# Optimization experiments

Measured on AMD Instinct MI355X. Metric: run time of the kernel, lower is better.

Reference implementation:

```python
import jax, jax.numpy as jnp
import numpy as np

DT = 0.1
B_SZ = 8192
T_HIST = 20
LEN_PRED = 30
FEAT = 32
N_LAYERS = 3
# state transition for constant-acceleration model (matches self.F in torch)
F_MAT = np.array([[1.0, DT, DT * DT / 2], [0.0, 1.0, DT], [0.0, 0.0, 1.0]], dtype=np.float32)


def setup_inputs() -> dict:
    key = jax.random.key(0)
    ks = jax.random.split(key, 16)
    # random-walk trajectories as history observations
    hist = jnp.cumsum(jax.random.normal(ks[0], (B_SZ, T_HIST, 2), jnp.float32) * 0.5, axis=1)
    k_lin = 1.0 / np.sqrt(FEAT)
    k_in = 1.0 / np.sqrt(24)

    def u(k, shape, scale):
        return jax.random.uniform(k, shape, jnp.float32, -scale, scale)

    return {
        "hist": hist,
        "max_accel_x": jnp.ones((1,), jnp.float32) * 10.0,
        "max_accel_y": jnp.ones((1,), jnp.float32) * 20.0,
        "velocity_std_x": jnp.ones((1,), jnp.float32) * 10.0,
        "acceleration_std_x": jnp.ones((1,), jnp.float32) * 10.0,
        "R_x_": jnp.array([0.0448], jnp.float32),
        "R_y_": jnp.array([0.001], jnp.float32),
        "G_x": jnp.array([0.0059, 0.2981, 0.0393], jnp.float32),
        "G_y": jnp.array([0.0059, 0.2981, 0.0393], jnp.float32) / 5.0,
        "Win_W": u(ks[1], (FEAT, 24), k_in),
        "Win_b": u(ks[2], (FEAT,), k_in),
        "enc_Wih": u(ks[3], (N_LAYERS, 4 * FEAT, FEAT), k_lin),
        "enc_Whh": u(ks[4], (N_LAYERS, 4 * FEAT, FEAT), k_lin),
        "enc_bih": u(ks[5], (N_LAYERS, 4 * FEAT), k_lin),
        "enc_bhh": u(ks[6], (N_LAYERS, 4 * FEAT), k_lin),
        "dec_Wih": u(ks[7], (N_LAYERS, 4 * FEAT, FEAT), k_lin),
        "dec_Whh": u(ks[8], (N_LAYERS, 4 * FEAT, FEAT), k_lin),
        "dec_bih": u(ks[9], (N_LAYERS, 4 * FEAT), k_lin),
        "dec_bhh": u(ks[10], (N_LAYERS, 4 * FEAT), k_lin),
        "Wout_W": u(ks[11], (4, FEAT), k_lin),
        "Wout_b": u(ks[12], (4,), k_lin),
        "len_pred": LEN_PRED,
    }


def reference(hist, max_accel_x, max_accel_y, velocity_std_x, acceleration_std_x,
              R_x_, R_y_, G_x, G_y, Win_W, Win_b,
              enc_Wih, enc_Whh, enc_bih, enc_bhh,
              dec_Wih, dec_Whh, dec_bih, dec_bhh,
              Wout_W, Wout_b, len_pred):
    B = hist.shape[0]
    F = jnp.asarray(F_MAT)
    R_x = R_x_[0] * R_x_[0]
    R_y = R_y_[0] * R_y_[0]
    Z_x = hist[:, :, 0]
    Z_y = hist[:, :, 1]

    def lstm(x, h, c, Wih, Whh, bih, bhh):
        g = x @ Wih.T + bih + h @ Whh.T + bhh
        i, f, gg, o = jnp.split(g, 4, axis=1)
        c = jax.nn.sigmoid(f) * c + jax.nn.sigmoid(i) * jnp.tanh(gg)
        h = jax.nn.sigmoid(o) * jnp.tanh(c)
        return h, c

    def stack(XP, h, c, Wih, Whh, bih, bhh):
        x = jnp.tanh(XP @ Win_W.T + Win_b)
        hs, cs = [], []
        for j in range(N_LAYERS):
            hj, cj = lstm(x, h[j], c[j], Wih[j], Whh[j], bih[j], bhh[j])
            hs.append(hj)
            cs.append(cj)
            x = cj  # torch code feeds the fresh CELL state to the next layer
        return jnp.stack(hs), jnp.stack(cs)

    def kpred(X, P, Q):
        return X @ F.T, jnp.einsum('ij,bjk,lk->bil', F, P, F) + Q

    def kupdate(X, P, z, R):
        y = z - X[:, 0]                      # innovation (H picks component 0)
        S = P[:, 0, 0] + R                   # innovation covariance (scalar)
        K = P[:, :, 0] / S[:, None]          # Kalman gain (B,3)
        return X + y[:, None] * K, P - K[:, :, None] * P[:, 0:1, :]

    def kinit(z0):
        # torch always calls _kalman_init with is_x=True (default), so both
        # axes use R_x / velocity_std_x / acceleration_std_x
        X = jnp.zeros((B, 3), hist.dtype).at[:, 0].set(z0)
        d = jnp.stack([R_x, velocity_std_x[0] ** 2, acceleration_std_x[0] ** 2])
        P = jnp.zeros((B, 3, 3), hist.dtype).at[:, jnp.arange(3), jnp.arange(3)].set(d)
        return X, P

    Qx_e = jnp.outer(G_x * max_accel_x[0], G_x * max_accel_x[0])
    Qy_e = jnp.outer(G_y * max_accel_y[0], G_y * max_accel_y[0])

    Xx, Px = kinit(Z_x[:, 0])
    Xy, Py = kinit(Z_y[:, 0])
    h = jnp.zeros((N_LAYERS, B, FEAT), hist.dtype)
    c = jnp.zeros_like(h)

    def enc_step(carry, zs):
        Xx, Px, Xy, Py, h, c = carry
        zx, zy = zs
        XP = jnp.concatenate([Xx, Xy, Px.reshape(B, 9), Py.reshape(B, 9)], 1)
        h, c = stack(XP, h, c, enc_Wih, enc_Whh, enc_bih, enc_bhh)
        Xx, Px = kpred(Xx, Px, Qx_e)
        Xy, Py = kpred(Xy, Py, Qy_e)
        Xx, Px = kupdate(Xx, Px, zx, R_x)
        Xy, Py = kupdate(Xy, Py, zy, R_y)
        return (Xx, Px, Xy, Py, h, c), None

    carry, _ = jax.lax.scan(enc_step, (Xx, Px, Xy, Py, h, c),
                            (Z_x[:, 1:].T, Z_y[:, 1:].T))

    oxx = jnp.outer(G_x, G_x)
    oyy = jnp.outer(G_y, G_y)

    def dec_step(carry, _):
        Xx, Px, Xy, Py, h, c = carry
        XP = jnp.concatenate([Xx, Xy, Px.reshape(B, 9), Py.reshape(B, 9)], 1)
        h, c = stack(XP, h, c, dec_Wih, dec_Whh, dec_bih, dec_bhh)
        pred = c[-1] @ Wout_W.T + Wout_b  # (B,4): [u_x, u_y, std_x, std_y]
        Xx = Xx.at[:, 2].set(DT * pred[:, 0])  # X[:,2] = B*u
        Xy = Xy.at[:, 2].set(DT * pred[:, 1])
        Qx = (pred[:, 2] ** 2)[:, None, None] * oxx
        Qy = (pred[:, 3] ** 2)[:, None, None] * oyy
        Xx, Px = kpred(Xx, Px, Qx)
        Xy, Py = kpred(Xy, Py, Qy)
        out = jnp.stack([Xx[:, 0], Xy[:, 0],
                         jnp.sqrt(Px[:, 0, 0]), jnp.sqrt(Py[:, 0, 0]),
                         jnp.zeros(B, hist.dtype)], axis=1)  # (B,5)
        return (Xx, Px, Xy, Py, h, c), out

    carry, ys = jax.lax.scan(dec_step, carry, None, length=len_pred)
    return jnp.transpose(ys, (1, 0, 2))  # (B, len_pred, 5)
```

## Files before the change

### kernel.cpp

```cpp
#include <hip/hip_runtime.h>
#include <math.h>

#define DT   0.1f
#define HDT  0.005f
#define T_HIST 20
#define LEN_PRED 30

typedef __attribute__((ext_vector_type(8))) short bfrag8;
typedef __attribute__((ext_vector_type(4))) float f32x4;

#define WS_FRAG   0u
#define WS_WIN    98304u
#define WS_WOUT   100352u
#define WS_BIAS   101376u

static __device__ __forceinline__ unsigned short f2bf(float x) {
    union { float f; unsigned int u; } v; v.f = x;
    unsigned int r = v.u + 0x7fffu + ((v.u >> 16) & 1u);
    return (unsigned short)(r >> 16);
}

static __device__ __forceinline__ unsigned int cvtpk(float lo, float hi) {
    unsigned int r;
    asm("v_cvt_pk_bf16_f32 %0, %1, %2" : "=v"(r) : "v"(lo), "v"(hi));
    return r;
}

__global__ void prep_kernel(const float* __restrict__ Win_W,
                            const float* __restrict__ eWih, const float* __restrict__ eWhh,
                            const float* __restrict__ ebih, const float* __restrict__ ebhh,
                            const float* __restrict__ dWih, const float* __restrict__ dWhh,
                            const float* __restrict__ dbih, const float* __restrict__ dbhh,
                            const float* __restrict__ Wout_W,
                            char* __restrict__ ws)
{
    int i = blockIdx.x * blockDim.x + threadIdx.x;
    if (i < 49152) {
        int fi = i >> 9, within = i & 511;
        int lane = within >> 3, jj = within & 7;
        int t = fi & 7, c = (fi >> 3) & 1;
        int pl = fi >> 4;
        int l = pl % 3, ph = pl / 3;
        int p = lane & 15, q2 = lane >> 4;
        int gate = p & 3;
        int feat = 8 * (p >> 2) + t;
        int row = gate * 32 + feat;
        int k = q2 * 8 + jj;
        const float* W = (c == 0) ? (ph ? dWih : eWih) : (ph ? dWhh : eWhh);
        ((unsigned short*)(ws + WS_FRAG))[i] = f2bf(W[l * 4096 + row * 32 + k]);
    } else if (i < 50176) {
        int i2 = i - 49152;
        int t = i2 >> 9, within = i2 & 511;
        int lane = within >> 3, jj = within & 7;
        int p = lane & 15, q2 = lane >> 4;
        int feat = 8 * (p >> 2) + 4 * t + (p & 3);
        int k = q2 * 8 + jj;
        float v = (k < 24) ? Win_W[feat * 24 + k] : 0.f;
        ((unsigned short*)(ws + WS_WIN))[i2] = f2bf(v);
    } else if (i < 50688) {
        int i3 = i - 50176;
        int lane = i3 >> 3, jj = i3 & 7;
        int p = lane & 15, q2 = lane >> 4;
        float v = Wout_W[(p & 3) * 32 + q2 * 8 + jj];
        ((unsigned short*)(ws + WS_WOUT))[i3] = f2bf(v);
    } else if (i < 51456) {
        int b = i - 50688;
        int ph = b / 384, rem = b % 384;
        int l = rem >> 7, w2 = rem & 127;
        int col = w2 >> 2, r = w2 & 3;
        const float* bi = ph ? dbih : ebih;
        const float* bh = ph ? dbhh : ebhh;
        ((float*)(ws + WS_BIAS))[b] = bi[l * 128 + r * 32 + col] + bh[l * 128 + r * 32 + col];
    }
}

__launch_bounds__(256, 2)
__global__ void kalman_lstm_kernel(const float* __restrict__ hist,
                                   const float* __restrict__ max_ax, const float* __restrict__ max_ay,
                                   const float* __restrict__ vstd, const float* __restrict__ astd,
                                   const float* __restrict__ Rx_, const float* __restrict__ Ry_,
                                   const float* __restrict__ Gx, const float* __restrict__ Gy,
                                   const float* __restrict__ Win_b, const float* __restrict__ Wout_b,
                                   const char* __restrict__ ws, float* __restrict__ out)
{
    __shared__ __align__(16) unsigned int xchC[3][2][4][16][4];
    __shared__ __align__(16) unsigned int xchH[3][2][4][16][4];
    __shared__ __align__(16) bfrag8 xenc[T_HIST - 1][64];

    const int tid  = threadIdx.x;
    const int wv   = tid >> 6;
    const int lane = tid & 63;
    const int q    = lane >> 4;
    const int m    = lane & 15;
    const int be   = blockIdx.x * 16 + m;
    const f32x4 zero4 = {0.f, 0.f, 0.f, 0.f};

    const bfrag8* fragp = (const bfrag8*)(ws + WS_FRAG);
    const f32x4*  biasp = (const f32x4*)(ws + WS_BIAS);

    bfrag8 fragA[3][2][2];
    f32x4  biasV[3][2];
    auto load_phase = [&](int ph) {
#pragma unroll
        for (int l = 0; l < 3; ++l) {
#pragma unroll
            for (int c = 0; c < 2; ++c)
#pragma unroll
                for (int j = 0; j < 2; ++j)
                    fragA[l][c][j] = fragp[(((ph * 3 + l) * 2 + c) * 8 + (2 * wv + j)) * 64 + lane];
#pragma unroll
            for (int j = 0; j < 2; ++j)
                biasV[l][j] = biasp[ph * 96 + l * 32 + (8 * q + 2 * wv + j)];
        }
    };

    bfrag8 winF0 = ((const bfrag8*)(ws + WS_WIN))[lane];
    bfrag8 winF1 = ((const bfrag8*)(ws + WS_WIN))[64 + lane];
    f32x4 winBv[2];
#pragma unroll
    for (int t = 0; t < 2; ++t)
#pragma unroll
        for (int r = 0; r < 4; ++r) winBv[t][r] = Win_b[8 * q + 4 * t + r];
    bfrag8 woutF = ((const bfrag8*)(ws + WS_WOUT))[lane];
    const float wb0 = Wout_b[0], wb1 = Wout_b[1], wb2 = Wout_b[2], wb3 = Wout_b[3];

    const float rx = Rx_[0] * Rx_[0], ry = Ry_[0] * Ry_[0];
    const float gX0 = Gx[0], gX1 = Gx[1], gX2 = Gx[2];
    const float gY0 = Gy[0], gY1 = Gy[1], gY2 = Gy[2];
    const float gx00 = gX0*gX0, gx01 = gX0*gX1, gx02 = gX0*gX2,
                gx11 = gX1*gX1, gx12 = gX1*gX2, gx22 = gX2*gX2;
    const float gy00 = gY0*gY0, gy01 = gY0*gY1, gy02 = gY0*gY2,
                gy11 = gY1*gY1, gy12 = gY1*gY2, gy22 = gY2*gY2;
    const float sx2 = max_ax[0] * max_ax[0], sy2 = max_ay[0] * max_ay[0];

    float Xx0 = hist[be * 40 + 0], Xx1 = 0.f, Xx2 = 0.f;
    float Xy0 = hist[be * 40 + 1], Xy1 = 0.f, Xy2 = 0.f;
    const float pv = vstd[0] * vstd[0], pa = astd[0] * astd[0];
    float Px00 = rx, Px01 = 0.f, Px02 = 0.f, Px11 = pv, Px12 = 0.f, Px22 = pa;
    float Py00 = rx, Py01 = 0.f, Py02 = 0.f, Py11 = pv, Py12 = 0.f, Py22 = pa;

    float creg[3][2];
#pragma unroll
    for (int l = 0; l < 3; ++l) { creg[l][0] = 0.f; creg[l][1] = 0.f; }

    auto sig = [](float z) { return __builtin_amdgcn_rcpf(1.f + __expf(-z)); };
    auto th  = [](float z) { return fmaf(-2.f, __builtin_amdgcn_rcpf(__expf(2.f * z) + 1.f), 1.f); };

    auto kpred9 = [](float& X0, float& X1, float& X2,
                     float& P00, float& P01, float& P02, float& P11, float& P12, float& P22,
                     float Q00, float Q01, float Q02, float Q11, float Q12, float Q22) {
        X0 = X0 + DT * X1 + HDT * X2;
        X1 = X1 + DT * X2;
        float M00 = P00 + DT * P01 + HDT * P02;
        float M01 = P01 + DT * P11 + HDT * P12;
        float M02 = P02 + DT * P12 + HDT * P22;
        float M11 = P11 + DT * P12;
        float M12 = P12 + DT * P22;
        float M22 = P22;
        P00 = M00 + DT * M01 + HDT * M02 + Q00;
        P01 = M01 + DT * M02 + Q01;
        P02 = M02 + Q02;
        P11 = M11 + DT * M12 + Q11;
        P12 = M12 + Q12;
        P22 = M22 + Q22;
    };
    auto kupd9 = [](float& X0, float& X1, float& X2,
                    float& P00, float& P01, float& P02, float& P11, float& P12, float& P22,
                    float z, float R) {
        float y = z - X0;
        float Sinv = 1.0f / (P00 + R);
        float K0 = P00 * Sinv, K1 = P01 * Sinv, K2 = P02 * Sinv;
        X0 += y * K0; X1 += y * K1; X2 += y * K2;
        float p00 = P00, p01 = P01, p02 = P02;
        P00 = p00 - K0 * p00;
        P01 = p01 - K0 * p01;
        P02 = p02 - K0 * p02;
        P11 = P11 - K1 * p01;
        P12 = P12 - K1 * p02;
        P22 = P22 - K2 * p02;
    };
    auto kf_enc_step = [&](int s) {
        float zx = hist[be * 40 + s * 2], zy = hist[be * 40 + s * 2 + 1];
        kpred9(Xx0, Xx1, Xx2, Px00, Px01, Px02, Px11, Px12, Px22,
               gx00*sx2, gx01*sx2, gx02*sx2, gx11*sx2, gx12*sx2, gx22*sx2);
        kupd9 (Xx0, Xx1, Xx2, Px00, Px01, Px02, Px11, Px12, Px22, zx, rx);
        kpred9(Xy0, Xy1, Xy2, Py00, Py01, Py02, Py11, Py12, Py22,
               gy00*sy2, gy01*sy2, gy02*sy2, gy11*sy2, gy12*sy2, gy22*sy2);
        kupd9 (Xy0, Xy1, Xy2, Py00, Py01, Py02, Py11, Py12, Py22, zy, ry);
    };

    auto packf = [&](const float* v) {
        union { bfrag8 f; unsigned int u[4]; } u;
#pragma unroll
        for (int d = 0; d < 4; ++d) u.u[d] = cvtpk(v[2 * d], v[2 * d + 1]);
        return u.f;
    };
    auto build_xp = [&]() {
        float v[8];
        if (q == 0)      { v[0]=Xx0;  v[1]=Xx1;  v[2]=Xx2;  v[3]=Xy0;  v[4]=Xy1;  v[5]=Xy2;  v[6]=Px00; v[7]=Px01; }
        else if (q == 1) { v[0]=Px02; v[1]=Px01; v[2]=Px11; v[3]=Px12; v[4]=Px02; v[5]=Px12; v[6]=Px22; v[7]=Py00; }
        else if (q == 2) { v[0]=Py01; v[1]=Py02; v[2]=Py01; v[3]=Py11; v[4]=Py12; v[5]=Py02; v[6]=Py12; v[7]=Py22; }
        else             { v[0]=0.f; v[1]=0.f; v[2]=0.f; v[3]=0.f; v[4]=0.f; v[5]=0.f; v[6]=0.f; v[7]=0.f; }
        return packf(v);
    };
    auto win_x0 = [&](bfrag8 xpf) {
        f32x4 a0 = __builtin_amdgcn_mfma_f32_16x16x32_bf16(winF0, xpf, winBv[0], 0, 0, 0);
        f32x4 a1 = __builtin_amdgcn_mfma_f32_16x16x32_bf16(winF1, xpf, winBv[1], 0, 0, 0);
        float v[8] = { th(a0[0]), th(a0[1]), th(a0[2]), th(a0[3]),
                       th(a1[0]), th(a1[1]), th(a1[2]), th(a1[3]) };
        return packf(v);
    };

    auto lstm_cells = [&](int l, bfrag8 xf, bfrag8 hf, unsigned int& cdw, unsigned int& hdw) {
        float cj[2], hj[2];
#pragma unroll
        for (int j = 0; j < 2; ++j) {
            f32x4 a = __builtin_amdgcn_mfma_f32_16x16x32_bf16(fragA[l][1][j], hf, biasV[l][j], 0, 0, 0);
            a = __builtin_amdgcn_mfma_f32_16x16x32_bf16(fragA[l][0][j], xf, a, 0, 0, 0);
            float iv = sig(a[0]), fv = sig(a[1]), gv = th(a[2]), ov = sig(a[3]);
            float c = fmaf(fv, creg[l][j], iv * gv);
            creg[l][j] = c;
            cj[j] = c;
            hj[j] = ov * th(c);
        }
        cdw = cvtpk(cj[0], cj[1]);
        hdw = cvtpk(hj[0], hj[1]);
    };

    bfrag8 c2f = bfrag8{};
    auto do_pred = [&](int tout) {
        f32x4 ap = __builtin_amdgcn_mfma_f32_16x16x32_bf16(woutF, c2f, zero4, 0, 0, 0);
        float p0 = ap[0] + wb0, p1 = ap[1] + wb1, p2 = ap[2] + wb2, p3 = ap[3] + wb3;
        Xx2 = DT * p0; Xy2 = DT * p1;
        float qsx = p2 * p2, qsy = p3 * p3;
        kpred9(Xx0, Xx1, Xx2, Px00, Px01, Px02, Px11, Px12, Px22,
               qsx*gx00, qsx*gx01, qsx*gx02, qsx*gx11, qsx*gx12, qsx*gx22);
        kpred9(Xy0, Xy1, Xy2, Py00, Py01, Py02, Py11, Py12, Py22,
               qsy*gy00, qsy*gy01, qsy*gy02, qsy*gy11, qsy*gy12, qsy*gy22);
        if (wv == 0 && q == 0) {
            float* o = out + (size_t)be * (LEN_PRED * 5) + tout * 5;
            o[0] = Xx0; o[1] = Xy0; o[2] = sqrtf(Px00); o[3] = sqrtf(Py00); o[4] = 0.f;
        }
    };

    for (int i = tid; i < 3 * 2 * 4 * 16 * 4; i += 256) {
        (&xchC[0][0][0][0][0])[i] = 0;
        (&xchH[0][0][0][0][0])[i] = 0;
    }

    load_phase(0);

#pragma unroll 1
    for (int s = 0; s < T_HIST - 1; ++s) {
        if (s > 0) kf_enc_step(s);
        bfrag8 x0f = win_x0(build_xp());
        if (wv == 0) xenc[s][lane] = x0f;
    }
    kf_enc_step(T_HIST - 1);
    __syncthreads();

#pragma unroll 1
    for (int p = 0; p < T_HIST + 1; ++p) {
        const int pw = p & 1, pr = pw ^ 1;
        const bool a0 = (p <= T_HIST - 2);
        const bool a1 = (p >= 1) && (p <= T_HIST - 1);
        const bool a2 = (p >= 2);
        unsigned int cd0, hd0, cd1, hd1, cd2, hd2;
        if (a0) {
            bfrag8 xf = xenc[p][lane];
            bfrag8 hf = *(const bfrag8*)&xchH[0][pr][q][m][0];
            lstm_cells(0, xf, hf, cd0, hd0);
        }
        if (a1) {
            bfrag8 xf = *(const bfrag8*)&xchC[0][pr][q][m][0];
            bfrag8 hf = *(const bfrag8*)&xchH[1][pr][q][m][0];
            lstm_cells(1, xf, hf, cd1, hd1);
        }
        if (a2) {
            bfrag8 xf = *(const bfrag8*)&xchC[1][pr][q][m][0];
            bfrag8 hf = *(const bfrag8*)&xchH[2][pr][q][m][0];
            lstm_cells(2, xf, hf, cd2, hd2);
        }
        if (a0) { xchC[0][pw][q][m][wv] = cd0; xchH[0][pw][q][m][wv] = hd0; }
        if (a1) { xchC[1][pw][q][m][wv] = cd1; xchH[1][pw][q][m][wv] = hd1; }
        if (a2) { xchC[2][pw][q][m][wv] = cd2; xchH[2][pw][q][m][wv] = hd2; }
        __syncthreads();
    }

    load_phase(1);
    bfrag8 hfragR[3];
    hfragR[0] = *(const bfrag8*)&xchH[0][0][q][m][0];
    hfragR[1] = *(const bfrag8*)&xchH[1][1][q][m][0];
    hfragR[2] = *(const bfrag8*)&xchH[2][0][q][m][0];
    c2f       = *(const bfrag8*)&xchC[2][0][q][m][0];
    __syncthreads();

#pragma unroll 1
    for (int t = 0; t < LEN_PRED; ++t) {
        if (t > 0) do_pred(t - 1);
        bfrag8 xf = win_x0(build_xp());
#pragma unroll
        for (int l = 0; l < 3; ++l) {
            unsigned int cdw, hdw;
            lstm_cells(l, xf, hfragR[l], cdw, hdw);
            xchC[l][0][q][m][wv] = cdw;
            xchH[l][0][q][m][wv] = hdw;
            __syncthreads();
            xf        = *(const bfrag8*)&xchC[l][0][q][m][0];
            hfragR[l] = *(const bfrag8*)&xchH[l][0][q][m][0];
        }
        c2f = xf;
    }
    do_pred(LEN_PRED - 1);
}

extern "C" void kernel_launch(void* const* d_in, const int* in_sizes, int n_in,
                              void* d_out, int out_size, void* d_ws, size_t ws_size,
                              hipStream_t stream)
{
    const float* hist  = (const float*)d_in[0];
    const float* maxax = (const float*)d_in[1];
    const float* maxay = (const float*)d_in[2];
    const float* vstd  = (const float*)d_in[3];
    const float* astd  = (const float*)d_in[4];
    const float* Rx    = (const float*)d_in[5];
    const float* Ry    = (const float*)d_in[6];
    const float* Gx    = (const float*)d_in[7];
    const float* Gy    = (const float*)d_in[8];
    const float* WinW  = (const float*)d_in[9];
    const float* Winb  = (const float*)d_in[10];
    const float* eWih  = (const float*)d_in[11];
    const float* eWhh  = (const float*)d_in[12];
    const float* ebih  = (const float*)d_in[13];
    const float* ebhh  = (const float*)d_in[14];
    const float* dWih  = (const float*)d_in[15];
    const float* dWhh  = (const float*)d_in[16];
    const float* dbih  = (const float*)d_in[17];
    const float* dbhh  = (const float*)d_in[18];
    const float* WoutW = (const float*)d_in[19];
    const float* Woutb = (const float*)d_in[20];
    char* ws = (char*)d_ws;
    float* out = (float*)d_out;

    prep_kernel<<<202, 256, 0, stream>>>(WinW, eWih, eWhh, ebih, ebhh,
                                         dWih, dWhh, dbih, dbhh, WoutW, ws);
    kalman_lstm_kernel<<<512, 256, 0, stream>>>(hist, maxax, maxay, vstd, astd,
                                                Rx, Ry, Gx, Gy, Winb, Woutb,
                                                ws, out);
}
```

Measured before the change: 193.4 us.

## Split Kalman x/y filters across waves, prescale gates for exp2, precompute hidden MFMAs

```diff
diff --git a/kernel.cpp b/kernel.cpp
--- a/kernel.cpp
+++ b/kernel.cpp
@@ -5,9 +5,12 @@
 #define HDT  0.005f
 #define T_HIST 20
 #define LEN_PRED 30
+#define L2E   1.4426950408889634f
+#define L2E2  2.8853900817779268f
 
 typedef __attribute__((ext_vector_type(8))) short bfrag8;
 typedef __attribute__((ext_vector_type(4))) float f32x4;
+typedef __attribute__((ext_vector_type(2))) unsigned int u32x2;
 
 #define WS_FRAG   0u
 #define WS_WIN    98304u
@@ -25,6 +28,8 @@
     asm("v_cvt_pk_bf16_f32 %0, %1, %2" : "=v"(r) : "v"(lo), "v"(hi));
     return r;
 }
+
+static __device__ __forceinline__ float ve2(float x) { return exp2f(x); }
 
 __global__ void prep_kernel(const float* __restrict__ Win_W,
                             const float* __restrict__ eWih, const float* __restrict__ eWhh,
@@ -46,16 +51,16 @@
         int feat = 8 * (p >> 2) + t;
         int row = gate * 32 + feat;
         int k = q2 * 8 + jj;
+        float s = (gate == 2) ? L2E2 : L2E;
         const float* W = (c == 0) ? (ph ? dWih : eWih) : (ph ? dWhh : eWhh);
-        ((unsigned short*)(ws + WS_FRAG))[i] = f2bf(W[l * 4096 + row * 32 + k]);
+        ((unsigned short*)(ws + WS_FRAG))[i] = f2bf(W[l * 4096 + row * 32 + k] * s);
     } else if (i < 50176) {
         int i2 = i - 49152;
-        int t = i2 >> 9, within = i2 & 511;
+        int w = i2 >> 9, within = i2 & 511;
         int lane = within >> 3, jj = within & 7;
         int p = lane & 15, q2 = lane >> 4;
-        int feat = 8 * (p >> 2) + 4 * t + (p & 3);
         int k = q2 * 8 + jj;
-        float v = (k < 24) ? Win_W[feat * 24 + k] : 0.f;
+        float v = (k < 24) ? Win_W[(w * 16 + p) * 24 + k] * L2E2 : 0.f;
         ((unsigned short*)(ws + WS_WIN))[i2] = f2bf(v);
     } else if (i < 50688) {
         int i3 = i - 50176;
@@ -68,9 +73,10 @@
         int ph = b / 384, rem = b % 384;
         int l = rem >> 7, w2 = rem & 127;
         int col = w2 >> 2, r = w2 & 3;
+        float s = (r == 2) ? L2E2 : L2E;
         const float* bi = ph ? dbih : ebih;
         const float* bh = ph ? dbhh : ebhh;
-        ((float*)(ws + WS_BIAS))[b] = bi[l * 128 + r * 32 + col] + bh[l * 128 + r * 32 + col];
+        ((float*)(ws + WS_BIAS))[b] = (bi[l * 128 + r * 32 + col] + bh[l * 128 + r * 32 + col]) * s;
     }
 }
 
@@ -85,7 +91,9 @@
 {
     __shared__ __align__(16) unsigned int xchC[3][2][4][16][4];
     __shared__ __align__(16) unsigned int xchH[3][2][4][16][4];
-    __shared__ __align__(16) bfrag8 xenc[T_HIST - 1][64];
+    __shared__ __align__(16) unsigned int xenc[T_HIST - 1][4][16][4];
+    __shared__ __align__(16) unsigned int x0b[4][16][4];
+    __shared__ __align__(16) unsigned int xps[2][4][16][4];
 
     const int tid  = threadIdx.x;
     const int wv   = tid >> 6;
@@ -113,42 +121,46 @@
                 biasV[l][j] = biasp[ph * 96 + l * 32 + (8 * q + 2 * wv + j)];
         }
     };
-
-    bfrag8 winF0 = ((const bfrag8*)(ws + WS_WIN))[lane];
-    bfrag8 winF1 = ((const bfrag8*)(ws + WS_WIN))[64 + lane];
-    f32x4 winBv[2];
-#pragma unroll
-    for (int t = 0; t < 2; ++t)
-#pragma unroll
-        for (int r = 0; r < 4; ++r) winBv[t][r] = Win_b[8 * q + 4 * t + r];
+    load_phase(0);
+
+    const int w  = (wv >= 2) ? (wv - 2) : 0;
+    const int ch = q & 1;
+    bfrag8 winF = ((const bfrag8*)(ws + WS_WIN))[w * 64 + lane];
+    f32x4 winBv;
+#pragma unroll
+    for (int r = 0; r < 4; ++r) winBv[r] = Win_b[w * 16 + q * 4 + r] * L2E2;
     bfrag8 woutF = ((const bfrag8*)(ws + WS_WOUT))[lane];
     const float wb0 = Wout_b[0], wb1 = Wout_b[1], wb2 = Wout_b[2], wb3 = Wout_b[3];
 
-    const float rx = Rx_[0] * Rx_[0], ry = Ry_[0] * Ry_[0];
-    const float gX0 = Gx[0], gX1 = Gx[1], gX2 = Gx[2];
-    const float gY0 = Gy[0], gY1 = Gy[1], gY2 = Gy[2];
-    const float gx00 = gX0*gX0, gx01 = gX0*gX1, gx02 = gX0*gX2,
-                gx11 = gX1*gX1, gx12 = gX1*gX2, gx22 = gX2*gX2;
-    const float gy00 = gY0*gY0, gy01 = gY0*gY1, gy02 = gY0*gY2,
-                gy11 = gY1*gY1, gy12 = gY1*gY2, gy22 = gY2*gY2;
-    const float sx2 = max_ax[0] * max_ax[0], sy2 = max_ay[0] * max_ay[0];
-
-    float Xx0 = hist[be * 40 + 0], Xx1 = 0.f, Xx2 = 0.f;
-    float Xy0 = hist[be * 40 + 1], Xy1 = 0.f, Xy2 = 0.f;
-    const float pv = vstd[0] * vstd[0], pa = astd[0] * astd[0];
-    float Px00 = rx, Px01 = 0.f, Px02 = 0.f, Px11 = pv, Px12 = 0.f, Px22 = pa;
-    float Py00 = rx, Py01 = 0.f, Py02 = 0.f, Py11 = pv, Py12 = 0.f, Py22 = pa;
+    float Rch = 0.f;
+    float g00 = 0.f, g01 = 0.f, g02 = 0.f, g11 = 0.f, g12 = 0.f, g22 = 0.f;
+    float e00 = 0.f, e01 = 0.f, e02 = 0.f, e11 = 0.f, e12 = 0.f, e22 = 0.f;
+    float X0 = 0.f, X1 = 0.f, X2 = 0.f;
+    float P00 = 0.f, P01 = 0.f, P02 = 0.f, P11 = 0.f, P12 = 0.f, P22 = 0.f;
+    if (wv >= 2) {
+        const float rx = Rx_[0] * Rx_[0], ry = Ry_[0] * Ry_[0];
+        Rch = ch ? ry : rx;
+        float G0, G1, G2, sc;
+        if (ch == 0) { G0 = Gx[0]; G1 = Gx[1]; G2 = Gx[2]; sc = max_ax[0]; }
+        else         { G0 = Gy[0]; G1 = Gy[1]; G2 = Gy[2]; sc = max_ay[0]; }
+        g00 = G0 * G0; g01 = G0 * G1; g02 = G0 * G2;
+        g11 = G1 * G1; g12 = G1 * G2; g22 = G2 * G2;
+        float s2 = sc * sc;
+        e00 = g00 * s2; e01 = g01 * s2; e02 = g02 * s2;
+        e11 = g11 * s2; e12 = g12 * s2; e22 = g22 * s2;
+        X0 = hist[be * 40 + ch];
+        P00 = rx; P11 = vstd[0] * vstd[0]; P22 = astd[0] * astd[0];
+    }
 
     float creg[3][2];
 #pragma unroll
     for (int l = 0; l < 3; ++l) { creg[l][0] = 0.f; creg[l][1] = 0.f; }
 
-    auto sig = [](float z) { return __builtin_amdgcn_rcpf(1.f + __expf(-z)); };
-    auto th  = [](float z) { return fmaf(-2.f, __builtin_amdgcn_rcpf(__expf(2.f * z) + 1.f), 1.f); };
-
-    auto kpred9 = [](float& X0, float& X1, float& X2,
-                     float& P00, float& P01, float& P02, float& P11, float& P12, float& P22,
-                     float Q00, float Q01, float Q02, float Q11, float Q12, float Q22) {
+    auto sig2 = [&](float z) { return __builtin_amdgcn_rcpf(1.f + ve2(-z)); };
+    auto th2  = [&](float z) { return fmaf(-2.f, __builtin_amdgcn_rcpf(ve2(z) + 1.f), 1.f); };
+    auto thc  = [&](float c) { return th2(c * L2E2); };
+
+    auto kpredL = [&](float Q00, float Q01, float Q02, float Q11, float Q12, float Q22) {
         X0 = X0 + DT * X1 + HDT * X2;
         X1 = X1 + DT * X2;
         float M00 = P00 + DT * P01 + HDT * P02;
@@ -164,11 +176,9 @@
         P12 = M12 + Q12;
         P22 = M22 + Q22;
     };
-    auto kupd9 = [](float& X0, float& X1, float& X2,
-                    float& P00, float& P01, float& P02, float& P11, float& P12, float& P22,
-                    float z, float R) {
+    auto kupdL = [&](float z) {
         float y = z - X0;
-        float Sinv = 1.0f / (P00 + R);
+        float Sinv = 1.0f / (P00 + Rch);
         float K0 = P00 * Sinv, K1 = P01 * Sinv, K2 = P02 * Sinv;
         X0 += y * K0; X1 += y * K1; X2 += y * K2;
         float p00 = P00, p01 = P01, p02 = P02;
@@ -180,67 +190,29 @@
         P22 = P22 - K2 * p02;
     };
     auto kf_enc_step = [&](int s) {
-        float zx = hist[be * 40 + s * 2], zy = hist[be * 40 + s * 2 + 1];
-        kpred9(Xx0, Xx1, Xx2, Px00, Px01, Px02, Px11, Px12, Px22,
-               gx00*sx2, gx01*sx2, gx02*sx2, gx11*sx2, gx12*sx2, gx22*sx2);
-        kupd9 (Xx0, Xx1, Xx2, Px00, Px01, Px02, Px11, Px12, Px22, zx, rx);
-        kpred9(Xy0, Xy1, Xy2, Py00, Py01, Py02, Py11, Py12, Py22,
-               gy00*sy2, gy01*sy2, gy02*sy2, gy11*sy2, gy12*sy2, gy22*sy2);
-        kupd9 (Xy0, Xy1, Xy2, Py00, Py01, Py02, Py11, Py12, Py22, zy, ry);
-    };
-
-    auto packf = [&](const float* v) {
-        union { bfrag8 f; unsigned int u[4]; } u;
-#pragma unroll
-        for (int d = 0; d < 4; ++d) u.u[d] = cvtpk(v[2 * d], v[2 * d + 1]);
-        return u.f;
-    };
-    auto build_xp = [&]() {
-        float v[8];
-        if (q == 0)      { v[0]=Xx0;  v[1]=Xx1;  v[2]=Xx2;  v[3]=Xy0;  v[4]=Xy1;  v[5]=Xy2;  v[6]=Px00; v[7]=Px01; }
-        else if (q == 1) { v[0]=Px02; v[1]=Px01; v[2]=Px11; v[3]=Px12; v[4]=Px02; v[5]=Px12; v[6]=Px22; v[7]=Py00; }
-        else if (q == 2) { v[0]=Py01; v[1]=Py02; v[2]=Py01; v[3]=Py11; v[4]=Py12; v[5]=Py02; v[6]=Py12; v[7]=Py22; }
-        else             { v[0]=0.f; v[1]=0.f; v[2]=0.f; v[3]=0.f; v[4]=0.f; v[5]=0.f; v[6]=0.f; v[7]=0.f; }
-        return packf(v);
-    };
-    auto win_x0 = [&](bfrag8 xpf) {
-        f32x4 a0 = __builtin_amdgcn_mfma_f32_16x16x32_bf16(winF0, xpf, winBv[0], 0, 0, 0);
-        f32x4 a1 = __builtin_amdgcn_mfma_f32_16x16x32_bf16(winF1, xpf, winBv[1], 0, 0, 0);
-        float v[8] = { th(a0[0]), th(a0[1]), th(a0[2]), th(a0[3]),
-                       th(a1[0]), th(a1[1]), th(a1[2]), th(a1[3]) };
-        return packf(v);
-    };
-
-    auto lstm_cells = [&](int l, bfrag8 xf, bfrag8 hf, unsigned int& cdw, unsigned int& hdw) {
-        float cj[2], hj[2];
-#pragma unroll
-        for (int j = 0; j < 2; ++j) {
-            f32x4 a = __builtin_amdgcn_mfma_f32_16x16x32_bf16(fragA[l][1][j], hf, biasV[l][j], 0, 0, 0);
-            a = __builtin_amdgcn_mfma_f32_16x16x32_bf16(fragA[l][0][j], xf, a, 0, 0, 0);
-            float iv = sig(a[0]), fv = sig(a[1]), gv = th(a[2]), ov = sig(a[3]);
-            float c = fmaf(fv, creg[l][j], iv * gv);
-            creg[l][j] = c;
-            cj[j] = c;
-            hj[j] = ov * th(c);
-        }
-        cdw = cvtpk(cj[0], cj[1]);
-        hdw = cvtpk(hj[0], hj[1]);
-    };
-
-    bfrag8 c2f = bfrag8{};
-    auto do_pred = [&](int tout) {
-        f32x4 ap = __builtin_amdgcn_mfma_f32_16x16x32_bf16(woutF, c2f, zero4, 0, 0, 0);
-        float p0 = ap[0] + wb0, p1 = ap[1] + wb1, p2 = ap[2] + wb2, p3 = ap[3] + wb3;
-        Xx2 = DT * p0; Xy2 = DT * p1;
-        float qsx = p2 * p2, qsy = p3 * p3;
-        kpred9(Xx0, Xx1, Xx2, Px00, Px01, Px02, Px11, Px12, Px22,
-               qsx*gx00, qsx*gx01, qsx*gx02, qsx*gx11, qsx*gx12, qsx*gx22);
-        kpred9(Xy0, Xy1, Xy2, Py00, Py01, Py02, Py11, Py12, Py22,
-               qsy*gy00, qsy*gy01, qsy*gy02, qsy*gy11, qsy*gy12, qsy*gy22);
-        if (wv == 0 && q == 0) {
-            float* o = out + (size_t)be * (LEN_PRED * 5) + tout * 5;
-            o[0] = Xx0; o[1] = Xy0; o[2] = sqrtf(Px00); o[3] = sqrtf(Py00); o[4] = 0.f;
-        }
+        float z = hist[be * 40 + s * 2 + ch];
+        kpredL(e00, e01, e02, e11, e12, e22);
+        kupdL(z);
+    };
+    auto stage_xp = [&]() {
+        if (q < 2) {
+            unsigned short* b = (unsigned short*)&xps[w][0][0][0];
+            auto wr = [&](int f, float v) { b[(f >> 3) * 128 + m * 8 + (f & 7)] = f2bf(v); };
+            int o = ch * 3;
+            wr(o + 0, X0); wr(o + 1, X1); wr(o + 2, X2);
+            int pb = 6 + ch * 9;
+            wr(pb + 0, P00); wr(pb + 1, P01); wr(pb + 2, P02);
+            wr(pb + 3, P01); wr(pb + 4, P11); wr(pb + 5, P12);
+            wr(pb + 6, P02); wr(pb + 7, P12); wr(pb + 8, P22);
+        }
+    };
+
+    auto gates_from = [&](int l, int j, f32x4 a, float& cv, float& hv) {
+        float iv = sig2(a[0]), fv = sig2(a[1]), gv = th2(a[2]), ov = sig2(a[3]);
+        float c = fmaf(fv, creg[l][j], iv * gv);
+        creg[l][j] = c;
+        cv = c;
+        hv = ov * thc(c);
     };
 
     for (int i = tid; i < 3 * 2 * 4 * 16 * 4; i += 256) {
@@ -248,42 +220,65 @@
         (&xchH[0][0][0][0][0])[i] = 0;
     }
 
-    load_phase(0);
-
+    if (wv >= 2) {
+        for (int i = lane; i < 4 * 16 * 4; i += 64) (&xps[w][0][0][0])[i] = 0;
 #pragma unroll 1
-    for (int s = 0; s < T_HIST - 1; ++s) {
-        if (s > 0) kf_enc_step(s);
-        bfrag8 x0f = win_x0(build_xp());
-        if (wv == 0) xenc[s][lane] = x0f;
-    }
-    kf_enc_step(T_HIST - 1);
+        for (int s = 0; s < T_HIST - 1; ++s) {
+            if (s > 0) kf_enc_step(s);
+            stage_xp();
+            bfrag8 bxp = *(const bfrag8*)&xps[w][q][m][0];
+            f32x4 aw = __builtin_amdgcn_mfma_f32_16x16x32_bf16(winF, bxp, winBv, 0, 0, 0);
+            float v0 = th2(aw[0]), v1 = th2(aw[1]), v2 = th2(aw[2]), v3 = th2(aw[3]);
+            u32x2 pk; pk.x = cvtpk(v0, v1); pk.y = cvtpk(v2, v3);
+            *(u32x2*)&xenc[s][2 * w + (q >> 1)][m][(q & 1) * 2] = pk;
+        }
+        kf_enc_step(T_HIST - 1);
+    }
     __syncthreads();
 
 #pragma unroll 1
     for (int p = 0; p < T_HIST + 1; ++p) {
         const int pw = p & 1, pr = pw ^ 1;
-        const bool a0 = (p <= T_HIST - 2);
-        const bool a1 = (p >= 1) && (p <= T_HIST - 1);
-        const bool a2 = (p >= 2);
+        const bool b0 = (p <= T_HIST - 2);
+        const bool b1 = (p >= 1) && (p <= T_HIST - 1);
+        const bool b2 = (p >= 2);
         unsigned int cd0, hd0, cd1, hd1, cd2, hd2;
-        if (a0) {
-            bfrag8 xf = xenc[p][lane];
+        if (b0) {
+            bfrag8 xf = *(const bfrag8*)&xenc[p][q][m][0];
             bfrag8 hf = *(const bfrag8*)&xchH[0][pr][q][m][0];
-            lstm_cells(0, xf, hf, cd0, hd0);
-        }
-        if (a1) {
+            f32x4 a = __builtin_amdgcn_mfma_f32_16x16x32_bf16(fragA[0][1][0], hf, biasV[0][0], 0, 0, 0);
+            a = __builtin_amdgcn_mfma_f32_16x16x32_bf16(fragA[0][0][0], xf, a, 0, 0, 0);
+            f32x4 b = __builtin_amdgcn_mfma_f32_16x16x32_bf16(fragA[0][1][1], hf, biasV[0][1], 0, 0, 0);
+            b = __builtin_amdgcn_mfma_f32_16x16x32_bf16(fragA[0][0][1], xf, b, 0, 0, 0);
+            float c0, h0, c1, h1;
+            gates_from(0, 0, a, c0, h0); gates_from(0, 1, b, c1, h1);
+            cd0 = cvtpk(c0, c1); hd0 = cvtpk(h0, h1);
+        }
+        if (b1) {
             bfrag8 xf = *(const bfrag8*)&xchC[0][pr][q][m][0];
             bfrag8 hf = *(const bfrag8*)&xchH[1][pr][q][m][0];
-            lstm_cells(1, xf, hf, cd1, hd1);
-        }
-        if (a2) {
+            f32x4 a = __builtin_amdgcn_mfma_f32_16x16x32_bf16(fragA[1][1][0], hf, biasV[1][0], 0, 0, 0);
+            a = __builtin_amdgcn_mfma_f32_16x16x32_bf16(fragA[1][0][0], xf, a, 0, 0, 0);
+            f32x4 b = __builtin_amdgcn_mfma_f32_16x16x32_bf16(fragA[1][1][1], hf, biasV[1][1], 0, 0, 0);
+            b = __builtin_amdgcn_mfma_f32_16x16x32_bf16(fragA[1][0][1], xf, b, 0, 0, 0);
+            float c0, h0, c1, h1;
+            gates_from(1, 0, a, c0, h0); gates_from(1, 1, b, c1, h1);
+            cd1 = cvtpk(c0, c1); hd1 = cvtpk(h0, h1);
+        }
+        if (b2) {
             bfrag8 xf = *(const bfrag8*)&xchC[1][pr][q][m][0];
             bfrag8 hf = *(const bfrag8*)&xchH[2][pr][q][m][0];
-            lstm_cells(2, xf, hf, cd2, hd2);
-        }
-        if (a0) { xchC[0][pw][q][m][wv] = cd0; xchH[0][pw][q][m][wv] = hd0; }
-        if (a1) { xchC[1][pw][q][m][wv] = cd1; xchH[1][pw][q][m][wv] = hd1; }
-        if (a2) { xchC[2][pw][q][m][wv] = cd2; xchH[2][pw][q][m][wv] = hd2; }
+            f32x4 a = __builtin_amdgcn_mfma_f32_16x16x32_bf16(fragA[2][1][0], hf, biasV[2][0], 0, 0, 0);
+            a = __builtin_amdgcn_mfma_f32_16x16x32_bf16(fragA[2][0][0], xf, a, 0, 0, 0);
+            f32x4 b = __builtin_amdgcn_mfma_f32_16x16x32_bf16(fragA[2][1][1], hf, biasV[2][1], 0, 0, 0);
+            b = __builtin_amdgcn_mfma_f32_16x16x32_bf16(fragA[2][0][1], xf, b, 0, 0, 0);
+            float c0, h0, c1, h1;
+            gates_from(2, 0, a, c0, h0); gates_from(2, 1, b, c1, h1);
+            cd2 = cvtpk(c0, c1); hd2 = cvtpk(h0, h1);
+        }
+        if (b0) { xchC[0][pw][q][m][wv] = cd0; xchH[0][pw][q][m][wv] = hd0; }
+        if (b1) { xchC[1][pw][q][m][wv] = cd1; xchH[1][pw][q][m][wv] = hd1; }
+        if (b2) { xchC[2][pw][q][m][wv] = cd2; xchH[2][pw][q][m][wv] = hd2; }
         __syncthreads();
     }
 
@@ -292,19 +287,52 @@
     hfragR[0] = *(const bfrag8*)&xchH[0][0][q][m][0];
     hfragR[1] = *(const bfrag8*)&xchH[1][1][q][m][0];
     hfragR[2] = *(const bfrag8*)&xchH[2][0][q][m][0];
-    c2f       = *(const bfrag8*)&xchC[2][0][q][m][0];
-    __syncthreads();
+    bfrag8 c2f = *(const bfrag8*)&xchC[2][0][q][m][0];
+
+    auto do_pred = [&](int tout) {
+        f32x4 ap = __builtin_amdgcn_mfma_f32_16x16x32_bf16(woutF, c2f, zero4, 0, 0, 0);
+        float pe = ch ? (ap[1] + wb1) : (ap[0] + wb0);
+        float qe = ch ? (ap[3] + wb3) : (ap[2] + wb2);
+        X2 = DT * pe;
+        float qs = qe * qe;
+        kpredL(qs * g00, qs * g01, qs * g02, qs * g11, qs * g12, qs * g22);
+        if (wv == 2 && q < 2) {
+            float* o = out + (size_t)be * (LEN_PRED * 5) + tout * 5;
+            if (ch == 0) { o[0] = X0; o[2] = sqrtf(P00); }
+            else         { o[1] = X0; o[3] = sqrtf(P00); o[4] = 0.f; }
+        }
+    };
 
 #pragma unroll 1
     for (int t = 0; t < LEN_PRED; ++t) {
-        if (t > 0) do_pred(t - 1);
-        bfrag8 xf = win_x0(build_xp());
+        f32x4 ah[3][2];
+#pragma unroll
+        for (int l = 0; l < 3; ++l)
+#pragma unroll
+            for (int j = 0; j < 2; ++j)
+                ah[l][j] = __builtin_amdgcn_mfma_f32_16x16x32_bf16(fragA[l][1][j], hfragR[l], biasV[l][j], 0, 0, 0);
+
+        if (wv >= 2) {
+            if (t > 0) do_pred(t - 1);
+            stage_xp();
+            bfrag8 bxp = *(const bfrag8*)&xps[w][q][m][0];
+            f32x4 aw = __builtin_amdgcn_mfma_f32_16x16x32_bf16(winF, bxp, winBv, 0, 0, 0);
+            float v0 = th2(aw[0]), v1 = th2(aw[1]), v2 = th2(aw[2]), v3 = th2(aw[3]);
+            u32x2 pk; pk.x = cvtpk(v0, v1); pk.y = cvtpk(v2, v3);
+            *(u32x2*)&x0b[2 * w + (q >> 1)][m][(q & 1) * 2] = pk;
+        }
+        __syncthreads();
+
+        bfrag8 xf = *(const bfrag8*)&x0b[q][m][0];
 #pragma unroll
         for (int l = 0; l < 3; ++l) {
-            unsigned int cdw, hdw;
-            lstm_cells(l, xf, hfragR[l], cdw, hdw);
-            xchC[l][0][q][m][wv] = cdw;
-            xchH[l][0][q][m][wv] = hdw;
+            f32x4 a0 = __builtin_amdgcn_mfma_f32_16x16x32_bf16(fragA[l][0][0], xf, ah[l][0], 0, 0, 0);
+            f32x4 a1 = __builtin_amdgcn_mfma_f32_16x16x32_bf16(fragA[l][0][1], xf, ah[l][1], 0, 0, 0);
+            float c0, h0, c1, h1;
+            gates_from(l, 0, a0, c0, h0);
+            gates_from(l, 1, a1, c1, h1);
+            xchC[l][0][q][m][wv] = cvtpk(c0, c1);
+            xchH[l][0][q][m][wv] = cvtpk(h0, h1);
             __syncthreads();
             xf        = *(const bfrag8*)&xchC[l][0][q][m][0];
             hfragR[l] = *(const bfrag8*)&xchH[l][0][q][m][0];
```

After: 207.3 us. +7.2%, slower.

## Split LSTM gate work across eight waves and specialize Kalman waves

Applied to the files above, without the earlier changes.

```diff
diff --git a/kernel.cpp b/kernel.cpp
--- a/kernel.cpp
+++ b/kernel.cpp
@@ -8,6 +8,7 @@
 
 typedef __attribute__((ext_vector_type(8))) short bfrag8;
 typedef __attribute__((ext_vector_type(4))) float f32x4;
+typedef __attribute__((ext_vector_type(2))) unsigned int u32x2;
 
 #define WS_FRAG   0u
 #define WS_WIN    98304u
@@ -43,19 +44,18 @@
         int l = pl % 3, ph = pl / 3;
         int p = lane & 15, q2 = lane >> 4;
         int gate = p & 3;
-        int feat = 8 * (p >> 2) + t;
+        int feat = (t >> 1) * 8 + 2 * (p >> 2) + (t & 1);
         int row = gate * 32 + feat;
         int k = q2 * 8 + jj;
         const float* W = (c == 0) ? (ph ? dWih : eWih) : (ph ? dWhh : eWhh);
         ((unsigned short*)(ws + WS_FRAG))[i] = f2bf(W[l * 4096 + row * 32 + k]);
     } else if (i < 50176) {
         int i2 = i - 49152;
-        int t = i2 >> 9, within = i2 & 511;
+        int w = i2 >> 9, within = i2 & 511;
         int lane = within >> 3, jj = within & 7;
         int p = lane & 15, q2 = lane >> 4;
-        int feat = 8 * (p >> 2) + 4 * t + (p & 3);
         int k = q2 * 8 + jj;
-        float v = (k < 24) ? Win_W[feat * 24 + k] : 0.f;
+        float v = (k < 24) ? Win_W[(w * 16 + p) * 24 + k] : 0.f;
         ((unsigned short*)(ws + WS_WIN))[i2] = f2bf(v);
     } else if (i < 50688) {
         int i3 = i - 50176;
@@ -74,7 +74,7 @@
     }
 }
 
-__launch_bounds__(256, 2)
+__launch_bounds__(512, 4)
 __global__ void kalman_lstm_kernel(const float* __restrict__ hist,
                                    const float* __restrict__ max_ax, const float* __restrict__ max_ay,
                                    const float* __restrict__ vstd, const float* __restrict__ astd,
@@ -85,7 +85,8 @@
 {
     __shared__ __align__(16) unsigned int xchC[3][2][4][16][4];
     __shared__ __align__(16) unsigned int xchH[3][2][4][16][4];
-    __shared__ __align__(16) bfrag8 xenc[T_HIST - 1][64];
+    __shared__ __align__(16) unsigned int xenc[T_HIST - 1][4][16][4];
+    __shared__ __align__(16) unsigned int x0b[4][16][4];
 
     const int tid  = threadIdx.x;
     const int wv   = tid >> 6;
@@ -98,29 +99,24 @@
     const bfrag8* fragp = (const bfrag8*)(ws + WS_FRAG);
     const f32x4*  biasp = (const f32x4*)(ws + WS_BIAS);
 
-    bfrag8 fragA[3][2][2];
-    f32x4  biasV[3][2];
+    bfrag8 fragA[3][2];
+    f32x4  biasV[3];
     auto load_phase = [&](int ph) {
 #pragma unroll
         for (int l = 0; l < 3; ++l) {
 #pragma unroll
             for (int c = 0; c < 2; ++c)
-#pragma unroll
-                for (int j = 0; j < 2; ++j)
-                    fragA[l][c][j] = fragp[(((ph * 3 + l) * 2 + c) * 8 + (2 * wv + j)) * 64 + lane];
-#pragma unroll
-            for (int j = 0; j < 2; ++j)
-                biasV[l][j] = biasp[ph * 96 + l * 32 + (8 * q + 2 * wv + j)];
-        }
-    };
-
-    bfrag8 winF0 = ((const bfrag8*)(ws + WS_WIN))[lane];
-    bfrag8 winF1 = ((const bfrag8*)(ws + WS_WIN))[64 + lane];
-    f32x4 winBv[2];
-#pragma unroll
-    for (int t = 0; t < 2; ++t)
-#pragma unroll
-        for (int r = 0; r < 4; ++r) winBv[t][r] = Win_b[8 * q + 4 * t + r];
+                fragA[l][c] = fragp[(((ph * 3 + l) * 2 + c) * 8 + wv) * 64 + lane];
+            biasV[l] = biasp[ph * 96 + l * 32 + ((wv >> 1) * 8 + 2 * q + (wv & 1))];
+        }
+    };
+    load_phase(0);
+
+    const int w = (wv >= 6) ? (wv - 6) : 0;
+    bfrag8 winF = ((const bfrag8*)(ws + WS_WIN))[w * 64 + lane];
+    f32x4 winBv;
+#pragma unroll
+    for (int r = 0; r < 4; ++r) winBv[r] = Win_b[w * 16 + q * 4 + r];
     bfrag8 woutF = ((const bfrag8*)(ws + WS_WOUT))[lane];
     const float wb0 = Wout_b[0], wb1 = Wout_b[1], wb2 = Wout_b[2], wb3 = Wout_b[3];
 
@@ -132,16 +128,18 @@
     const float gy00 = gY0*gY0, gy01 = gY0*gY1, gy02 = gY0*gY2,
                 gy11 = gY1*gY1, gy12 = gY1*gY2, gy22 = gY2*gY2;
     const float sx2 = max_ax[0] * max_ax[0], sy2 = max_ay[0] * max_ay[0];
+    const float ex00 = gx00*sx2, ex01 = gx01*sx2, ex02 = gx02*sx2,
+                ex11 = gx11*sx2, ex12 = gx12*sx2, ex22 = gx22*sx2;
+    const float ey00 = gy00*sy2, ey01 = gy01*sy2, ey02 = gy02*sy2,
+                ey11 = gy11*sy2, ey12 = gy12*sy2, ey22 = gy22*sy2;
+    const float pv = vstd[0] * vstd[0], pa = astd[0] * astd[0];
 
     float Xx0 = hist[be * 40 + 0], Xx1 = 0.f, Xx2 = 0.f;
     float Xy0 = hist[be * 40 + 1], Xy1 = 0.f, Xy2 = 0.f;
-    const float pv = vstd[0] * vstd[0], pa = astd[0] * astd[0];
     float Px00 = rx, Px01 = 0.f, Px02 = 0.f, Px11 = pv, Px12 = 0.f, Px22 = pa;
     float Py00 = rx, Py01 = 0.f, Py02 = 0.f, Py11 = pv, Py12 = 0.f, Py22 = pa;
 
-    float creg[3][2];
-#pragma unroll
-    for (int l = 0; l < 3; ++l) { creg[l][0] = 0.f; creg[l][1] = 0.f; }
+    float creg[3] = {0.f, 0.f, 0.f};
 
     auto sig = [](float z) { return __builtin_amdgcn_rcpf(1.f + __expf(-z)); };
     auto th  = [](float z) { return fmaf(-2.f, __builtin_amdgcn_rcpf(__expf(2.f * z) + 1.f), 1.f); };
@@ -181,11 +179,9 @@
     };
     auto kf_enc_step = [&](int s) {
         float zx = hist[be * 40 + s * 2], zy = hist[be * 40 + s * 2 + 1];
-        kpred9(Xx0, Xx1, Xx2, Px00, Px01, Px02, Px11, Px12, Px22,
-               gx00*sx2, gx01*sx2, gx02*sx2, gx11*sx2, gx12*sx2, gx22*sx2);
+        kpred9(Xx0, Xx1, Xx2, Px00, Px01, Px02, Px11, Px12, Px22, ex00, ex01, ex02, ex11, ex12, ex22);
         kupd9 (Xx0, Xx1, Xx2, Px00, Px01, Px02, Px11, Px12, Px22, zx, rx);
-        kpred9(Xy0, Xy1, Xy2, Py00, Py01, Py02, Py11, Py12, Py22,
-               gy00*sy2, gy01*sy2, gy02*sy2, gy11*sy2, gy12*sy2, gy22*sy2);
+        kpred9(Xy0, Xy1, Xy2, Py00, Py01, Py02, Py11, Py12, Py22, ey00, ey01, ey02, ey11, ey12, ey22);
         kupd9 (Xy0, Xy1, Xy2, Py00, Py01, Py02, Py11, Py12, Py22, zy, ry);
     };
 
@@ -203,28 +199,26 @@
         else             { v[0]=0.f; v[1]=0.f; v[2]=0.f; v[3]=0.f; v[4]=0.f; v[5]=0.f; v[6]=0.f; v[7]=0.f; }
         return packf(v);
     };
-    auto win_x0 = [&](bfrag8 xpf) {
-        f32x4 a0 = __builtin_amdgcn_mfma_f32_16x16x32_bf16(winF0, xpf, winBv[0], 0, 0, 0);
-        f32x4 a1 = __builtin_amdgcn_mfma_f32_16x16x32_bf16(winF1, xpf, winBv[1], 0, 0, 0);
-        float v[8] = { th(a0[0]), th(a0[1]), th(a0[2]), th(a0[3]),
-                       th(a1[0]), th(a1[1]), th(a1[2]), th(a1[3]) };
-        return packf(v);
-    };
-
-    auto lstm_cells = [&](int l, bfrag8 xf, bfrag8 hf, unsigned int& cdw, unsigned int& hdw) {
-        float cj[2], hj[2];
-#pragma unroll
-        for (int j = 0; j < 2; ++j) {
-            f32x4 a = __builtin_amdgcn_mfma_f32_16x16x32_bf16(fragA[l][1][j], hf, biasV[l][j], 0, 0, 0);
-            a = __builtin_amdgcn_mfma_f32_16x16x32_bf16(fragA[l][0][j], xf, a, 0, 0, 0);
-            float iv = sig(a[0]), fv = sig(a[1]), gv = th(a[2]), ov = sig(a[3]);
-            float c = fmaf(fv, creg[l][j], iv * gv);
-            creg[l][j] = c;
-            cj[j] = c;
-            hj[j] = ov * th(c);
-        }
-        cdw = cvtpk(cj[0], cj[1]);
-        hdw = cvtpk(hj[0], hj[1]);
+    auto win_emit = [&](unsigned int* dst) {
+        bfrag8 xpf = build_xp();
+        f32x4 aw = __builtin_amdgcn_mfma_f32_16x16x32_bf16(winF, xpf, winBv, 0, 0, 0);
+        u32x2 pk;
+        pk.x = cvtpk(th(aw[0]), th(aw[1]));
+        pk.y = cvtpk(th(aw[2]), th(aw[3]));
+        *(u32x2*)(dst + ((2 * w + (q >> 1)) * 16 + m) * 4 + (q & 1) * 2) = pk;
+    };
+
+    const int sidx = ((wv >> 1) * 16 + m) * 8 + 2 * q + (wv & 1);
+    auto cell = [&](int l, bfrag8 xf, bfrag8 hf, unsigned int* Cb, unsigned int* Hb) {
+        f32x4 a = __builtin_amdgcn_mfma_f32_16x16x32_bf16(fragA[l][1], hf, biasV[l], 0, 0, 0);
+        a = __builtin_amdgcn_mfma_f32_16x16x32_bf16(fragA[l][0], xf, a, 0, 0, 0);
+        float iv = sig(a[0]), fv = sig(a[1]), gv = th(a[2]), ov = sig(a[3]);
+        float c = fmaf(fv, creg[l], iv * gv);
+        creg[l] = c;
+        float h = ov * th(c);
+        unsigned int pk = cvtpk(c, h);
+        ((unsigned short*)Cb)[sidx] = (unsigned short)pk;
+        ((unsigned short*)Hb)[sidx] = (unsigned short)(pk >> 16);
     };
 
     bfrag8 c2f = bfrag8{};
@@ -237,53 +231,45 @@
                qsx*gx00, qsx*gx01, qsx*gx02, qsx*gx11, qsx*gx12, qsx*gx22);
         kpred9(Xy0, Xy1, Xy2, Py00, Py01, Py02, Py11, Py12, Py22,
                qsy*gy00, qsy*gy01, qsy*gy02, qsy*gy11, qsy*gy12, qsy*gy22);
-        if (wv == 0 && q == 0) {
+        if (wv == 6 && q == 0) {
             float* o = out + (size_t)be * (LEN_PRED * 5) + tout * 5;
             o[0] = Xx0; o[1] = Xy0; o[2] = sqrtf(Px00); o[3] = sqrtf(Py00); o[4] = 0.f;
         }
     };
 
-    for (int i = tid; i < 3 * 2 * 4 * 16 * 4; i += 256) {
+    for (int i = tid; i < 3 * 2 * 4 * 16 * 4; i += 512) {
         (&xchC[0][0][0][0][0])[i] = 0;
         (&xchH[0][0][0][0][0])[i] = 0;
     }
 
-    load_phase(0);
-
+    if (wv >= 6) {
 #pragma unroll 1
-    for (int s = 0; s < T_HIST - 1; ++s) {
-        if (s > 0) kf_enc_step(s);
-        bfrag8 x0f = win_x0(build_xp());
-        if (wv == 0) xenc[s][lane] = x0f;
-    }
-    kf_enc_step(T_HIST - 1);
+        for (int s = 0; s < T_HIST - 1; ++s) {
+            if (s > 0) kf_enc_step(s);
+            win_emit(&xenc[s][0][0][0]);
+        }
+        kf_enc_step(T_HIST - 1);
+    }
     __syncthreads();
 
 #pragma unroll 1
     for (int p = 0; p < T_HIST + 1; ++p) {
         const int pw = p & 1, pr = pw ^ 1;
-        const bool a0 = (p <= T_HIST - 2);
-        const bool a1 = (p >= 1) && (p <= T_HIST - 1);
-        const bool a2 = (p >= 2);
-        unsigned int cd0, hd0, cd1, hd1, cd2, hd2;
-        if (a0) {
-            bfrag8 xf = xenc[p][lane];
+        if (p <= T_HIST - 2) {
+            bfrag8 xf = *(const bfrag8*)&xenc[p][q][m][0];
             bfrag8 hf = *(const bfrag8*)&xchH[0][pr][q][m][0];
-            lstm_cells(0, xf, hf, cd0, hd0);
-        }
-        if (a1) {
+            cell(0, xf, hf, &xchC[0][pw][0][0][0], &xchH[0][pw][0][0][0]);
+        }
+        if (p >= 1 && p <= T_HIST - 1) {
             bfrag8 xf = *(const bfrag8*)&xchC[0][pr][q][m][0];
             bfrag8 hf = *(const bfrag8*)&xchH[1][pr][q][m][0];
-            lstm_cells(1, xf, hf, cd1, hd1);
-        }
-        if (a2) {
+            cell(1, xf, hf, &xchC[1][pw][0][0][0], &xchH[1][pw][0][0][0]);
+        }
+        if (p >= 2) {
             bfrag8 xf = *(const bfrag8*)&xchC[1][pr][q][m][0];
             bfrag8 hf = *(const bfrag8*)&xchH[2][pr][q][m][0];
-            lstm_cells(2, xf, hf, cd2, hd2);
-        }
-        if (a0) { xchC[0][pw][q][m][wv] = cd0; xchH[0][pw][q][m][wv] = hd0; }
-        if (a1) { xchC[1][pw][q][m][wv] = cd1; xchH[1][pw][q][m][wv] = hd1; }
-        if (a2) { xchC[2][pw][q][m][wv] = cd2; xchH[2][pw][q][m][wv] = hd2; }
+            cell(2, xf, hf, &xchC[2][pw][0][0][0], &xchH[2][pw][0][0][0]);
+        }
         __syncthreads();
     }
 
@@ -293,25 +279,38 @@
     hfragR[1] = *(const bfrag8*)&xchH[1][1][q][m][0];
     hfragR[2] = *(const bfrag8*)&xchH[2][0][q][m][0];
     c2f       = *(const bfrag8*)&xchC[2][0][q][m][0];
-    __syncthreads();
 
 #pragma unroll 1
     for (int t = 0; t < LEN_PRED; ++t) {
-        if (t > 0) do_pred(t - 1);
-        bfrag8 xf = win_x0(build_xp());
+        f32x4 ah[3];
+#pragma unroll
+        for (int l = 0; l < 3; ++l)
+            ah[l] = __builtin_amdgcn_mfma_f32_16x16x32_bf16(fragA[l][1], hfragR[l], biasV[l], 0, 0, 0);
+
+        if (wv >= 6) {
+            if (t > 0) do_pred(t - 1);
+            win_emit(&x0b[0][0][0]);
+        }
+        __syncthreads();
+
+        bfrag8 xf = *(const bfrag8*)&x0b[q][m][0];
 #pragma unroll
         for (int l = 0; l < 3; ++l) {
-            unsigned int cdw, hdw;
-            lstm_cells(l, xf, hfragR[l], cdw, hdw);
-            xchC[l][0][q][m][wv] = cdw;
-            xchH[l][0][q][m][wv] = hdw;
+            f32x4 a = __builtin_amdgcn_mfma_f32_16x16x32_bf16(fragA[l][0], xf, ah[l], 0, 0, 0);
+            float iv = sig(a[0]), fv = sig(a[1]), gv = th(a[2]), ov = sig(a[3]);
+            float c = fmaf(fv, creg[l], iv * gv);
+            creg[l] = c;
+            float h = ov * th(c);
+            unsigned int pk = cvtpk(c, h);
+            ((unsigned short*)&xchC[l][0][0][0][0])[sidx] = (unsigned short)pk;
+            ((unsigned short*)&xchH[l][0][0][0][0])[sidx] = (unsigned short)(pk >> 16);
             __syncthreads();
             xf        = *(const bfrag8*)&xchC[l][0][q][m][0];
             hfragR[l] = *(const bfrag8*)&xchH[l][0][q][m][0];
         }
         c2f = xf;
     }
-    do_pred(LEN_PRED - 1);
+    if (wv >= 6) do_pred(LEN_PRED - 1);
 }
 
 extern "C" void kernel_launch(void* const* d_in, const int* in_sizes, int n_in,
@@ -344,7 +343,7 @@
 
     prep_kernel<<<202, 256, 0, stream>>>(WinW, eWih, eWhh, ebih, ebhh,
                                          dWih, dWhh, dbih, dbhh, WoutW, ws);
-    kalman_lstm_kernel<<<512, 256, 0, stream>>>(hist, maxax, maxay, vstd, astd,
+    kalman_lstm_kernel<<<512, 512, 0, stream>>>(hist, maxax, maxay, vstd, astd,
                                                 Rx, Ry, Gx, Gy, Winb, Woutb,
                                                 ws, out);
 }
```

After: 197.4 us. +2.1%, slower.
